# Kernel tuning notes

Hardware: AMD Instinct MI355X
Metric: run time of the kernel (lower is better)

Reference implementation:

```python
import jax, jax.numpy as jnp
import numpy as np

B, W, F_IN = 128, 128, 64   # batch, window_size, num_features
N = 64                      # nodes per graph == num_features == tcn_out_channels
E = 4096                    # edges per graph
ED = 16                     # edge_feature_dim
H, C = 4, 32                # heads, gat_out_dim
FLAT = N * H * C            # 8192
HID = FLAT // 4             # 2048
LRELU_SLOPE = 0.01          # F.leaky_relu default
BN_EPS = 1e-5


def setup_inputs() -> dict:
    key = jax.random.key(0)
    ks = jax.random.split(key, 16)
    x = jax.random.normal(ks[0], (B, W, F_IN), jnp.float32)
    edge_index = jax.random.randint(ks[1], (2, E), 0, N)
    edge_attr = jax.random.normal(ks[2], (B, E, ED), jnp.float32)
    s = lambda k, shape, fan: jax.random.normal(k, shape, jnp.float32) / np.sqrt(fan)
    tcn_w = s(ks[3], (N, F_IN, 3), F_IN * 3)
    tcn_b = jnp.zeros((N,), jnp.float32)
    lin_l_w = s(ks[4], (H * C, W), W)
    lin_l_b = jnp.zeros((H * C,), jnp.float32)
    lin_e_w = s(ks[5], (H * C, ED), ED)
    lin_e_b = jnp.zeros((H * C,), jnp.float32)
    att = s(ks[6], (1, H, C), C)
    fc1_w = s(ks[7], (HID, FLAT), FLAT)
    fc1_b = jnp.zeros((HID,), jnp.float32)
    bn_g = jnp.ones((HID,), jnp.float32)
    bn_b = jnp.zeros((HID,), jnp.float32)
    fc2_w = s(ks[8], (2, HID), HID)
    fc2_b = jnp.zeros((2,), jnp.float32)
    return dict(x=x, edge_index=edge_index, edge_attr=edge_attr,
                tcn_w=tcn_w, tcn_b=tcn_b,
                lin_l_w=lin_l_w, lin_l_b=lin_l_b,
                lin_e_w=lin_e_w, lin_e_b=lin_e_b, att=att,
                fc1_w=fc1_w, fc1_b=fc1_b, bn_g=bn_g, bn_b=bn_b,
                fc2_w=fc2_w, fc2_b=fc2_b)


def reference(x, edge_index, edge_attr, tcn_w, tcn_b,
              lin_l_w, lin_l_b, lin_e_w, lin_e_b, att,
              fc1_w, fc1_b, bn_g, bn_b, fc2_w, fc2_b):
    # TCN: Conv1d(k=3, pad=1) over the window dim
    xt = jnp.transpose(x, (0, 2, 1))  # [B, F_IN, W]
    x_g = jax.lax.conv_general_dilated(
        xt, tcn_w, window_strides=(1,), padding=((1, 1),),
        dimension_numbers=('NCH', 'OIH', 'NCH')) + tcn_b[None, :, None]
    # x_g: [B, N, W] -> per-sample graph with N nodes, W-dim node features

    src, dst = edge_index[0], edge_index[1]

    def gat_one(xn, ea):
        # xn: [N, W], ea: [E, ED]
        h = (xn @ lin_l_w.T + lin_l_b).reshape(N, H, C)
        e = (ea @ lin_e_w.T + lin_e_b).reshape(E, H, C)
        xi = h[dst]               # [E, H, C] target node feats
        xj = h[src]               # [E, H, C] source node feats
        a = jax.nn.leaky_relu(xi + xj + e, LRELU_SLOPE)
        score = jnp.einsum('ehc,ohc->eh', a, att)  # [E, H]
        # segment softmax over edges grouped by destination node
        m = jax.ops.segment_max(score, dst, num_segments=N)
        m = jnp.where(jnp.isfinite(m), m, 0.0)
        ex = jnp.exp(score - m[dst])
        den = jax.ops.segment_sum(ex, dst, num_segments=N)
        alpha = ex / (den[dst] + 1e-16)            # [E, H]
        msg = xj * alpha[:, :, None]               # [E, H, C]
        out = jax.ops.segment_sum(msg, dst, num_segments=N)  # [N, H, C]
        return out.reshape(N, H * C)

    x_gat = jax.vmap(gat_one)(x_g, edge_attr)      # [B, N, H*C]
    x_gat = jax.nn.elu(x_gat)
    x_flat = x_gat.reshape(B, FLAT)

    h1 = x_flat @ fc1_w.T + fc1_b
    # BatchNorm1d in eval mode with fresh running stats (mean=0, var=1)
    h1 = h1 * (bn_g / jnp.sqrt(1.0 + BN_EPS)) + bn_b
    h1 = jax.nn.relu(h1)  # dropout is identity in eval
    logits = h1 @ fc2_w.T + fc2_b
    return logits
```

## Files before the change

### kernel.cpp

```cpp
#include <hip/hip_runtime.h>
#include <math.h>

#define BB   128
#define WW   128
#define FIN  64
#define NNODE 64
#define NE   4096
#define EDIM 16
#define NH   4
#define CDIM 32
#define HC   128
#define FLATD 8192
#define HIDD 2048

#define OFF_H    0u
#define OFF_P    1048576u
#define OFF_XGB  3211264u
#define OFF_BK   4259840u

typedef unsigned short u16;
typedef u16      u16x8 __attribute__((ext_vector_type(8)));
typedef __bf16   bf16x8 __attribute__((ext_vector_type(8)));
typedef float    f32x4  __attribute__((ext_vector_type(4)));
typedef float    f32x16 __attribute__((ext_vector_type(16)));

__device__ __forceinline__ u16 f2bf(float f) {
    unsigned u = __float_as_uint(f);
    u += 0x7fffu + ((u >> 16) & 1u);
    return (u16)(u >> 16);
}
__device__ __forceinline__ void hilo(float v, u16* h, u16* l) {
    u16 hh = f2bf(v);
    float hf = __uint_as_float(((unsigned)hh) << 16);
    *h = hh;
    *l = f2bf(v - hf);
}

__global__ __launch_bounds__(256) void k01(
        const float* __restrict__ x, const float* __restrict__ tcn_w,
        const float* __restrict__ tcn_b, const float* __restrict__ lin_l_w,
        const float* __restrict__ lin_l_b, float* __restrict__ h,
        const int* __restrict__ ei, int* __restrict__ bstart,
        int* __restrict__ blist)
{
    __shared__ float xs[130*65];
    __shared__ float xg[32*132];
    __shared__ float twT[192*32];
    __shared__ int cnt[64];
    __shared__ int cur[65];
    const int bid = blockIdx.x, t = threadIdx.x;

    if (bid == 256) {
        if (t < 64) cnt[t] = 0;
        __syncthreads();
        for (int e = t; e < NE; e += 256) atomicAdd(&cnt[ei[NE + e]], 1);
        __syncthreads();
        if (t == 0) {
            int run = 0;
            for (int n = 0; n < 64; ++n) { cur[n] = run; run += cnt[n]; }
            cur[64] = run;
        }
        __syncthreads();
        if (t < 65) bstart[t] = cur[t];
        __syncthreads();
        for (int e = t; e < NE; e += 256) {
            int d = ei[NE + e], s = ei[e];
            int p = atomicAdd(&cur[d], 1);
            blist[p] = (e << 12) | (d << 6) | s;
        }
        return;
    }

    const int b = bid >> 1, half = bid & 1;
    const int n0 = half * 32;

    for (int idx = t; idx < 8192; idx += 256) {
        int w = idx >> 6, i = idx & 63;
        xs[(w+1)*65 + i] = x[b*8192 + idx];
    }
    for (int idx = t; idx < 6144; idx += 256) {
        const int nl = idx & 31, ik = idx >> 5;
        twT[idx] = tcn_w[(n0 + nl)*192 + ik];
    }
    if (t < 65) { xs[t] = 0.f; xs[129*65 + t] = 0.f; }
    __syncthreads();

    {
        const int nl = t >> 3;
        const int n  = n0 + nl;
        const int w0 = (t & 7) * 16;
        float acc[16];
        const float tb = tcn_b[n];
#pragma unroll
        for (int j = 0; j < 16; ++j) acc[j] = tb;
        for (int i = 0; i < 64; ++i) {
            const float t0 = twT[(3*i + 0)*32 + nl];
            const float t1 = twT[(3*i + 1)*32 + nl];
            const float t2 = twT[(3*i + 2)*32 + nl];
            float a = xs[(w0+0)*65 + i];
            float c0 = xs[(w0+1)*65 + i];
#pragma unroll
            for (int dw = 0; dw < 16; ++dw) {
                float c = xs[(w0+dw+2)*65 + i];
                acc[dw] += a*t0 + c0*t1 + c*t2;
                a = c0; c0 = c;
            }
        }
#pragma unroll
        for (int dw = 0; dw < 16; ++dw) xg[nl*132 + w0 + dw] = acc[dw];
    }
    __syncthreads();

    {
        const int o2 = t & 63, ng = t >> 6;
        const int oA = o2, oB = o2 + 64;
        float accA[8], accB[8];
        const float lbA = lin_l_b[oA], lbB = lin_l_b[oB];
#pragma unroll
        for (int j = 0; j < 8; ++j) { accA[j] = lbA; accB[j] = lbB; }
        for (int c = 0; c < 32; ++c) {
            const float4 lwA = *(const float4*)&lin_l_w[oA*128 + c*4];
            const float4 lwB = *(const float4*)&lin_l_w[oB*128 + c*4];
#pragma unroll
            for (int nn = 0; nn < 8; ++nn) {
                const float4 xv = *(const float4*)&xg[(ng*8+nn)*132 + c*4];
                accA[nn] += xv.x*lwA.x + xv.y*lwA.y + xv.z*lwA.z + xv.w*lwA.w;
                accB[nn] += xv.x*lwB.x + xv.y*lwB.y + xv.z*lwB.z + xv.w*lwB.w;
            }
        }
#pragma unroll
        for (int nn = 0; nn < 8; ++nn) {
            const int n = n0 + ng*8 + nn;
            h[(b*64 + n)*128 + oA] = accA[nn];
            h[(b*64 + n)*128 + oB] = accB[nn];
        }
    }
}

#define CAPF 2560
__global__ __launch_bounds__(512, 1) void k2_fused(
        const float* __restrict__ hbase, const float* __restrict__ ea,
        const float* __restrict__ lin_e_w, const float* __restrict__ lin_e_b,
        const float* __restrict__ att, const int* __restrict__ bstart,
        const int* __restrict__ blist, u16* __restrict__ xgb)
{
    __shared__ float hbuf[64*132];
    __shared__ float scl[CAPF*4];
    __shared__ float Pm[4][32][68];
    __shared__ int   bst[33];
    const int b = blockIdx.x, half = blockIdx.y, t = threadIdx.x;
    const int lane = t & 63, wv = t >> 6, l32 = lane & 31, h5 = lane >> 5;

    const int lo  = bstart[half*32];
    const int cnt = min(bstart[half*32 + 32] - lo, CAPF);
    const int gcnt = (cnt + 31) >> 5;

    int g = wv;
    int pkc = 0; bool validc = false;
    float4 v0c = {0.f,0.f,0.f,0.f}, v1c = {0.f,0.f,0.f,0.f};
    if (g < gcnt) {
        const int idx0 = g*32 + l32;
        validc = idx0 < cnt;
        pkc = validc ? blist[lo + idx0] : 0;
        const float* eap = ea + ((size_t)b*NE + (size_t)(pkc >> 12))*16 + h5*8;
        v0c = *(const float4*)eap;
        v1c = *(const float4*)(eap + 4);
    }

    for (int idx = t; idx < 2048; idx += 512) {
        const int row = idx >> 5, c4 = (idx & 31) * 4;
        float4 hv = *(const float4*)&hbase[(size_t)b*8192 + row*128 + c4];
        const float4 eb = *(const float4*)&lin_e_b[c4];
        hv.x += 0.5f*eb.x; hv.y += 0.5f*eb.y;
        hv.z += 0.5f*eb.z; hv.w += 0.5f*eb.w;
        *(float4*)&hbuf[row*132 + c4] = hv;
    }
    {
        const f32x4 z4 = {0.f, 0.f, 0.f, 0.f};
        for (int idx = t; idx < 4*32*68/4; idx += 512) ((f32x4*)Pm)[idx] = z4;
    }
    if (t < 33) bst[t] = bstart[half*32 + t];
    bf16x8 Ah[4], Al[4];
#pragma unroll
    for (int mt = 0; mt < 4; ++mt) {
        const float* wp = &lin_e_w[(mt*32 + l32)*16 + h5*8];
        const float4 w0 = *(const float4*)wp;
        const float4 w1 = *(const float4*)(wp + 4);
        u16 th[8], tl[8];
        hilo(w0.x,&th[0],&tl[0]); hilo(w0.y,&th[1],&tl[1]);
        hilo(w0.z,&th[2],&tl[2]); hilo(w0.w,&th[3],&tl[3]);
        hilo(w1.x,&th[4],&tl[4]); hilo(w1.y,&th[5],&tl[5]);
        hilo(w1.z,&th[6],&tl[6]); hilo(w1.w,&th[7],&tl[7]);
        u16x8 vh = { th[0],th[1],th[2],th[3],th[4],th[5],th[6],th[7] };
        u16x8 vl = { tl[0],tl[1],tl[2],tl[3],tl[4],tl[5],tl[6],tl[7] };
        Ah[mt] = *(bf16x8*)&vh;
        Al[mt] = *(bf16x8*)&vl;
    }
    float4 attv[4][4];
#pragma unroll
    for (int mt = 0; mt < 4; ++mt)
#pragma unroll
        for (int gq = 0; gq < 4; ++gq)
            attv[mt][gq] = *(const float4*)&att[mt*32 + gq*8 + h5*4];
    __syncthreads();

    while (g < gcnt) {
        const int gn = g + 8;
        const int pk = pkc; const bool valid = validc;
        const float4 v0 = v0c, v1 = v1c;
        const int idx = g*32 + l32;
        if (gn < gcnt) {
            const int idxn = gn*32 + l32;
            validc = idxn < cnt;
            pkc = validc ? blist[lo + idxn] : 0;
            const float* eap = ea + ((size_t)b*NE + (size_t)(pkc >> 12))*16 + h5*8;
            v0c = *(const float4*)eap;
            v1c = *(const float4*)(eap + 4);
        } else {
            validc = false;
        }
        const int sn = pk & 63, dd = (pk >> 6) & 63;
        u16 bh[8], bl[8];
        hilo(v0.x,&bh[0],&bl[0]); hilo(v0.y,&bh[1],&bl[1]);
        hilo(v0.z,&bh[2],&bl[2]); hilo(v0.w,&bh[3],&bl[3]);
        hilo(v1.x,&bh[4],&bl[4]); hilo(v1.y,&bh[5],&bl[5]);
        hilo(v1.z,&bh[6],&bl[6]); hilo(v1.w,&bh[7],&bl[7]);
        u16x8 vbh = { bh[0],bh[1],bh[2],bh[3],bh[4],bh[5],bh[6],bh[7] };
        u16x8 vbl = { bl[0],bl[1],bl[2],bl[3],bl[4],bl[5],bl[6],bl[7] };
        const bf16x8 Bh = *(bf16x8*)&vbh;
        const bf16x8 Bl = *(bf16x8*)&vbl;
        float hacc[4];
#pragma unroll
        for (int mt = 0; mt < 4; ++mt) {
            f32x16 D = {0.f,0.f,0.f,0.f,0.f,0.f,0.f,0.f,
                        0.f,0.f,0.f,0.f,0.f,0.f,0.f,0.f};
            D = __builtin_amdgcn_mfma_f32_32x32x16_bf16(Al[mt], Bh, D, 0, 0, 0);
            D = __builtin_amdgcn_mfma_f32_32x32x16_bf16(Ah[mt], Bl, D, 0, 0, 0);
            D = __builtin_amdgcn_mfma_f32_32x32x16_bf16(Ah[mt], Bh, D, 0, 0, 0);
            float s = 0.f;
#pragma unroll
            for (int g4 = 0; g4 < 4; ++g4) {
                const int ob = mt*32 + g4*8 + h5*4;
                const float4 hd = *(const float4*)&hbuf[dd*132 + ob];
                const float4 hs = *(const float4*)&hbuf[sn*132 + ob];
                float x0 = hd.x + hs.x + D[g4*4+0];
                float x1 = hd.y + hs.y + D[g4*4+1];
                float x2 = hd.z + hs.z + D[g4*4+2];
                float x3 = hd.w + hs.w + D[g4*4+3];
                x0 = fmaxf(x0, 0.01f*x0); x1 = fmaxf(x1, 0.01f*x1);
                x2 = fmaxf(x2, 0.01f*x2); x3 = fmaxf(x3, 0.01f*x3);
                const float4 a4 = attv[mt][g4];
                s += a4.x*x0 + a4.y*x1 + a4.z*x2 + a4.w*x3;
            }
            hacc[mt] = s;
        }
#pragma unroll
        for (int hh = 0; hh < 4; ++hh)
            hacc[hh] += __shfl_xor(hacc[hh], 32);
        if (h5 == 0 && valid)
            *(float4*)&scl[idx*4] = make_float4(hacc[0], hacc[1], hacc[2], hacc[3]);
        g = gn;
    }
    __syncthreads();

    {
        const int pair = t >> 2, sub = t & 3;
        const int nl = pair >> 2, hh = pair & 3;
        const int s0 = bst[nl] - lo, s1 = bst[nl+1] - lo;
        float mx = -3.4e38f;
        for (int i = s0 + sub; i < s1; i += 4) mx = fmaxf(mx, scl[i*4 + hh]);
        mx = fmaxf(mx, __shfl_xor(mx, 1));
        mx = fmaxf(mx, __shfl_xor(mx, 2));
        float den = 0.f;
        for (int i = s0 + sub; i < s1; i += 4) {
            const float ex = __expf(scl[i*4 + hh] - mx);
            scl[i*4 + hh] = ex;
            den += ex;
        }
        den += __shfl_xor(den, 1);
        den += __shfl_xor(den, 2);
        const float rd = 1.0f / (den + 1e-16f);
        for (int i = s0 + sub; i < s1; i += 4) {
            const int src = blist[lo + i] & 63;
            atomicAdd(&Pm[hh][nl][src], scl[i*4 + hh] * rd);
        }
    }
    __syncthreads();

    {
        const int hh = wv >> 1, ct = wv & 1;
        const int l16 = lane & 15, q = lane >> 4;
        const int cb = hh*32 + ct*16 + l16;
        const float lb2 = 0.5f * lin_e_b[cb];
        bf16x8 Hh2[2], Hl2[2];
#pragma unroll
        for (int kk = 0; kk < 2; ++kk) {
            u16 hhv[8], hlv[8];
#pragma unroll
            for (int i = 0; i < 8; ++i) {
                const float v = hbuf[(kk*32 + q*8 + i)*132 + cb];
                hilo(v, &hhv[i], &hlv[i]);
            }
            u16x8 vhh = { hhv[0],hhv[1],hhv[2],hhv[3],hhv[4],hhv[5],hhv[6],hhv[7] };
            u16x8 vhl = { hlv[0],hlv[1],hlv[2],hlv[3],hlv[4],hlv[5],hlv[6],hlv[7] };
            Hh2[kk] = *(bf16x8*)&vhh;
            Hl2[kk] = *(bf16x8*)&vhl;
        }
#pragma unroll
        for (int mrow = 0; mrow < 32; mrow += 16) {
            f32x4 D = {0.f, 0.f, 0.f, 0.f};
#pragma unroll
            for (int kk = 0; kk < 2; ++kk) {
                const float* pp = &Pm[hh][mrow + l16][kk*32 + q*8];
                const float4 a0 = *(const float4*)pp;
                const float4 a1 = *(const float4*)(pp + 4);
                u16 ph[8], pl[8];
                hilo(a0.x,&ph[0],&pl[0]); hilo(a0.y,&ph[1],&pl[1]);
                hilo(a0.z,&ph[2],&pl[2]); hilo(a0.w,&ph[3],&pl[3]);
                hilo(a1.x,&ph[4],&pl[4]); hilo(a1.y,&ph[5],&pl[5]);
                hilo(a1.z,&ph[6],&pl[6]); hilo(a1.w,&ph[7],&pl[7]);
                u16x8 vph = { ph[0],ph[1],ph[2],ph[3],ph[4],ph[5],ph[6],ph[7] };
                u16x8 vpl = { pl[0],pl[1],pl[2],pl[3],pl[4],pl[5],pl[6],pl[7] };
                const bf16x8 Ph = *(bf16x8*)&vph, Pl = *(bf16x8*)&vpl;
                D = __builtin_amdgcn_mfma_f32_16x16x32_bf16(Pl, Hh2[kk], D, 0, 0, 0);
                D = __builtin_amdgcn_mfma_f32_16x16x32_bf16(Ph, Hl2[kk], D, 0, 0, 0);
                D = __builtin_amdgcn_mfma_f32_16x16x32_bf16(Ph, Hh2[kk], D, 0, 0, 0);
            }
#pragma unroll
            for (int r = 0; r < 4; ++r) {
                const int m = mrow + q*4 + r;
                const float corr = (bst[m+1] > bst[m]) ? lb2 : 0.f;
                float v = D[r] - corr;
                v = v > 0.f ? v : expm1f(v);
                xgb[(size_t)b*8192 + (half*32 + m)*128 + cb] = f2bf(v);
            }
        }
    }
}

__global__ __launch_bounds__(256) void k3_fc1(
        const u16* __restrict__ xgb, const float* __restrict__ fc1_w,
        float* __restrict__ part)
{
    __shared__ u16 Ash[2][128*72];
    __shared__ u16 Bsh[2][32*72];
    const int jb = blockIdx.x, ks = blockIdx.y, t = threadIdx.x;
    const int j0 = jb*32, k0 = ks*1024;
    const int wave = t >> 6, lane = t & 63;
    const int quad = lane >> 4, l16 = lane & 15;
    const int wm = (wave & 1) * 64, wn = (wave >> 1) * 16;

    f32x4 acc[4];
#pragma unroll
    for (int i = 0; i < 4; ++i) acc[i] = (f32x4){0.f, 0.f, 0.f, 0.f};

    const int arow = t >> 1, acol = (t & 1) * 32;
    const int brow = t >> 3, bcol = (t & 7) * 8;

#define K3_LOAD(KC, AR, B0, B1)                                              \
    {   const u16* ap = xgb + (size_t)arow*FLATD + k0 + (KC) + acol;         \
        AR[0] = *(const u16x8*)(ap);      AR[1] = *(const u16x8*)(ap + 8);   \
        AR[2] = *(const u16x8*)(ap + 16); AR[3] = *(const u16x8*)(ap + 24);  \
        const float* bp = fc1_w + (size_t)(j0 + brow)*FLATD + k0 + (KC) + bcol; \
        B0 = *(const float4*)bp; B1 = *(const float4*)(bp + 4); }

#define K3_WRITE(BUF, AR, B0, B1)                                            \
    {   *(u16x8*)&Ash[BUF][arow*72 + acol]      = AR[0];                     \
        *(u16x8*)&Ash[BUF][arow*72 + acol + 8]  = AR[1];                     \
        *(u16x8*)&Ash[BUF][arow*72 + acol + 16] = AR[2];                     \
        *(u16x8*)&Ash[BUF][arow*72 + acol + 24] = AR[3];                     \
        u16x8 u = { f2bf(B0.x), f2bf(B0.y), f2bf(B0.z), f2bf(B0.w),          \
                    f2bf(B1.x), f2bf(B1.y), f2bf(B1.z), f2bf(B1.w) };        \
        *(u16x8*)&Bsh[BUF][brow*72 + bcol] = u; }

#define K3_MFMA(BUF)                                                         \
    {   _Pragma("unroll")                                                    \
        for (int kk = 0; kk < 64; kk += 32) {                                \
            bf16x8 af[4], bfr;                                               \
            _Pragma("unroll")                                                \
            for (int i = 0; i < 4; ++i)                                      \
                af[i] = *(const bf16x8*)&Ash[BUF][(wm + i*16 + l16)*72 + kk + quad*8]; \
            bfr = *(const bf16x8*)&Bsh[BUF][(wn + l16)*72 + kk + quad*8];    \
            _Pragma("unroll")                                                \
            for (int i = 0; i < 4; ++i)                                      \
                acc[i] = __builtin_amdgcn_mfma_f32_16x16x32_bf16(af[i], bfr, acc[i], 0, 0, 0); \
        } }

    u16x8 Ar0[4]; float4 B00, B01;
    u16x8 Ar1[4]; float4 B10, B11;

    K3_LOAD(0, Ar0, B00, B01);
    K3_WRITE(0, Ar0, B00, B01);
    K3_LOAD(64, Ar0, B00, B01);
    K3_LOAD(128, Ar1, B10, B11);
    __syncthreads();

    for (int kc = 0; kc < 1024; kc += 128) {
        K3_MFMA(0);
        if (kc + 64 < 1024)  K3_WRITE(1, Ar0, B00, B01);
        if (kc + 192 < 1024) K3_LOAD(kc + 192, Ar0, B00, B01);
        __syncthreads();
        K3_MFMA(1);
        if (kc + 128 < 1024) K3_WRITE(0, Ar1, B10, B11);
        if (kc + 256 < 1024) K3_LOAD(kc + 256, Ar1, B10, B11);
        __syncthreads();
    }
#undef K3_LOAD
#undef K3_WRITE
#undef K3_MFMA

#pragma unroll
    for (int i = 0; i < 4; ++i) {
        const int n = j0 + wn + l16;
#pragma unroll
        for (int r = 0; r < 4; ++r) {
            const int m = wm + i*16 + quad*4 + r;
            part[(size_t)ks*262144 + (size_t)m*HIDD + n] = acc[i][r];
        }
    }
}

__global__ __launch_bounds__(1024) void k4_fc2(
        const float* __restrict__ part, const float* __restrict__ fc1_b,
        const float* __restrict__ bn_g, const float* __restrict__ bn_b,
        const float* __restrict__ fc2_w, const float* __restrict__ fc2_b,
        float* __restrict__ out)
{
    __shared__ float w0s[16], w1s[16];
    const int b = blockIdx.x, t = threadIdx.x;
    const int lane = t & 63, wv = t >> 6;
    const float inv = 1.0f / sqrtf(1.0f + 1e-5f);
    float p0 = 0.f, p1 = 0.f;
#pragma unroll
    for (int jj = 0; jj < 2; ++jj) {
        const int j = t + jj*1024;
        float hv = 0.f;
#pragma unroll
        for (int s = 0; s < 8; ++s) hv += part[(size_t)s*262144 + (size_t)b*2048 + j];
        float v = (hv + fc1_b[j]) * (bn_g[j] * inv) + bn_b[j];
        v = fmaxf(v, 0.f);
        p0 += v * fc2_w[j];
        p1 += v * fc2_w[2048 + j];
    }
#pragma unroll
    for (int d = 1; d < 64; d <<= 1) {
        p0 += __shfl_xor(p0, d);
        p1 += __shfl_xor(p1, d);
    }
    if (lane == 0) { w0s[wv] = p0; w1s[wv] = p1; }
    __syncthreads();
    if (t == 0) {
        float s0 = 0.f, s1 = 0.f;
#pragma unroll
        for (int i = 0; i < 16; ++i) { s0 += w0s[i]; s1 += w1s[i]; }
        out[b*2 + 0] = s0 + fc2_b[0];
        out[b*2 + 1] = s1 + fc2_b[1];
    }
}

extern "C" void kernel_launch(void* const* d_in, const int* in_sizes, int n_in,
                              void* d_out, int out_size, void* d_ws, size_t ws_size,
                              hipStream_t stream)
{
    const float* x       = (const float*)d_in[0];
    const int*   ei      = (const int*)  d_in[1];
    const float* ea      = (const float*)d_in[2];
    const float* tcn_w   = (const float*)d_in[3];
    const float* tcn_b   = (const float*)d_in[4];
    const float* lin_l_w = (const float*)d_in[5];
    const float* lin_l_b = (const float*)d_in[6];
    const float* lin_e_w = (const float*)d_in[7];
    const float* lin_e_b = (const float*)d_in[8];
    const float* att     = (const float*)d_in[9];
    const float* fc1_w   = (const float*)d_in[10];
    const float* fc1_b   = (const float*)d_in[11];
    const float* bn_g    = (const float*)d_in[12];
    const float* bn_b    = (const float*)d_in[13];
    const float* fc2_w   = (const float*)d_in[14];
    const float* fc2_b   = (const float*)d_in[15];

    float* ws     = (float*)d_ws;
    float* hbuf   = ws + OFF_H;
    float* part   = ws + OFF_P;
    u16*   xgb    = (u16*)(ws + OFF_XGB);
    int*   bstart = (int*)(ws + OFF_BK);
    int*   blist  = bstart + 80;
    float* out    = (float*)d_out;

    k01    <<<257, 256, 0, stream>>>(x, tcn_w, tcn_b, lin_l_w, lin_l_b, hbuf,
                                     ei, bstart, blist);
    k2_fused<<<dim3(BB, 2), 512, 0, stream>>>(hbuf, ea, lin_e_w, lin_e_b, att,
                                              bstart, blist, xgb);
    k3_fc1 <<<dim3(64, 8), 256, 0, stream>>>(xgb, fc1_w, part);
    k4_fc2 <<<BB, 1024, 0, stream>>>(part, fc1_b, bn_g, bn_b, fc2_w, fc2_b, out);
}
```

Before: 232.3 us.

## Fuse TCN conv and node projection into GAT kernel, drop global h buffer

The TCN convolution and lin_l projection now run inside the GAT kernel, writing node features straight into shared memory through a union-style shared layout instead of round-tripping through a global buffer. Edge bucketing moves to its own single-block kernel. The aim is to remove the global write and re-read of h and the work split across two launches. The cost is that each of the two blocks per sample (one per half of the destination nodes) now recomputes the full 64-node conv and projection. It also adds 512 threads' worth of extra compute before the edge phase of a kernel that runs at one block per CU.

```diff
diff --git a/kernel.cpp b/kernel.cpp
--- a/kernel.cpp
+++ b/kernel.cpp
@@ -36,118 +36,57 @@
     *l = f2bf(v - hf);
 }
 
-__global__ __launch_bounds__(256) void k01(
+__global__ __launch_bounds__(256) void k0_bucket(
+        const int* __restrict__ ei, int* __restrict__ bstart, int* __restrict__ blist)
+{
+    __shared__ int cnt[64];
+    __shared__ int cur[65];
+    const int t = threadIdx.x;
+    if (t < 64) cnt[t] = 0;
+    __syncthreads();
+    for (int e = t; e < NE; e += 256) atomicAdd(&cnt[ei[NE + e]], 1);
+    __syncthreads();
+    if (t == 0) {
+        int run = 0;
+        for (int n = 0; n < 64; ++n) { cur[n] = run; run += cnt[n]; }
+        cur[64] = run;
+    }
+    __syncthreads();
+    if (t < 65) bstart[t] = cur[t];
+    __syncthreads();
+    for (int e = t; e < NE; e += 256) {
+        int d = ei[NE + e], s = ei[e];
+        int p = atomicAdd(&cur[d], 1);
+        blist[p] = (e << 12) | (d << 6) | s;
+    }
+}
+
+#define CAPF 2560
+#define SM_XG   0u
+#define SM_HB   33792u
+#define SM_XS   33792u
+#define SM_TWT  67600u
+#define SM_SCL  67600u
+#define SM_PM   108560u
+#define SM_BST  143376u
+#define SM_SZ   143512u
+__global__ __launch_bounds__(512, 1) void k2_fused(
         const float* __restrict__ x, const float* __restrict__ tcn_w,
         const float* __restrict__ tcn_b, const float* __restrict__ lin_l_w,
-        const float* __restrict__ lin_l_b, float* __restrict__ h,
-        const int* __restrict__ ei, int* __restrict__ bstart,
-        int* __restrict__ blist)
-{
-    __shared__ float xs[130*65];
-    __shared__ float xg[32*132];
-    __shared__ float twT[192*32];
-    __shared__ int cnt[64];
-    __shared__ int cur[65];
-    const int bid = blockIdx.x, t = threadIdx.x;
-
-    if (bid == 256) {
-        if (t < 64) cnt[t] = 0;
-        __syncthreads();
-        for (int e = t; e < NE; e += 256) atomicAdd(&cnt[ei[NE + e]], 1);
-        __syncthreads();
-        if (t == 0) {
-            int run = 0;
-            for (int n = 0; n < 64; ++n) { cur[n] = run; run += cnt[n]; }
-            cur[64] = run;
-        }
-        __syncthreads();
-        if (t < 65) bstart[t] = cur[t];
-        __syncthreads();
-        for (int e = t; e < NE; e += 256) {
-            int d = ei[NE + e], s = ei[e];
-            int p = atomicAdd(&cur[d], 1);
-            blist[p] = (e << 12) | (d << 6) | s;
-        }
-        return;
-    }
-
-    const int b = bid >> 1, half = bid & 1;
-    const int n0 = half * 32;
-
-    for (int idx = t; idx < 8192; idx += 256) {
-        int w = idx >> 6, i = idx & 63;
-        xs[(w+1)*65 + i] = x[b*8192 + idx];
-    }
-    for (int idx = t; idx < 6144; idx += 256) {
-        const int nl = idx & 31, ik = idx >> 5;
-        twT[idx] = tcn_w[(n0 + nl)*192 + ik];
-    }
-    if (t < 65) { xs[t] = 0.f; xs[129*65 + t] = 0.f; }
-    __syncthreads();
-
-    {
-        const int nl = t >> 3;
-        const int n  = n0 + nl;
-        const int w0 = (t & 7) * 16;
-        float acc[16];
-        const float tb = tcn_b[n];
-#pragma unroll
-        for (int j = 0; j < 16; ++j) acc[j] = tb;
-        for (int i = 0; i < 64; ++i) {
-            const float t0 = twT[(3*i + 0)*32 + nl];
-            const float t1 = twT[(3*i + 1)*32 + nl];
-            const float t2 = twT[(3*i + 2)*32 + nl];
-            float a = xs[(w0+0)*65 + i];
-            float c0 = xs[(w0+1)*65 + i];
-#pragma unroll
-            for (int dw = 0; dw < 16; ++dw) {
-                float c = xs[(w0+dw+2)*65 + i];
-                acc[dw] += a*t0 + c0*t1 + c*t2;
-                a = c0; c0 = c;
-            }
-        }
-#pragma unroll
-        for (int dw = 0; dw < 16; ++dw) xg[nl*132 + w0 + dw] = acc[dw];
-    }
-    __syncthreads();
-
-    {
-        const int o2 = t & 63, ng = t >> 6;
-        const int oA = o2, oB = o2 + 64;
-        float accA[8], accB[8];
-        const float lbA = lin_l_b[oA], lbB = lin_l_b[oB];
-#pragma unroll
-        for (int j = 0; j < 8; ++j) { accA[j] = lbA; accB[j] = lbB; }
-        for (int c = 0; c < 32; ++c) {
-            const float4 lwA = *(const float4*)&lin_l_w[oA*128 + c*4];
-            const float4 lwB = *(const float4*)&lin_l_w[oB*128 + c*4];
-#pragma unroll
-            for (int nn = 0; nn < 8; ++nn) {
-                const float4 xv = *(const float4*)&xg[(ng*8+nn)*132 + c*4];
-                accA[nn] += xv.x*lwA.x + xv.y*lwA.y + xv.z*lwA.z + xv.w*lwA.w;
-                accB[nn] += xv.x*lwB.x + xv.y*lwB.y + xv.z*lwB.z + xv.w*lwB.w;
-            }
-        }
-#pragma unroll
-        for (int nn = 0; nn < 8; ++nn) {
-            const int n = n0 + ng*8 + nn;
-            h[(b*64 + n)*128 + oA] = accA[nn];
-            h[(b*64 + n)*128 + oB] = accB[nn];
-        }
-    }
-}
-
-#define CAPF 2560
-__global__ __launch_bounds__(512, 1) void k2_fused(
-        const float* __restrict__ hbase, const float* __restrict__ ea,
+        const float* __restrict__ lin_l_b, const float* __restrict__ ea,
         const float* __restrict__ lin_e_w, const float* __restrict__ lin_e_b,
         const float* __restrict__ att, const int* __restrict__ bstart,
         const int* __restrict__ blist, u16* __restrict__ xgb)
 {
-    __shared__ float hbuf[64*132];
-    __shared__ float scl[CAPF*4];
-    __shared__ float Pm[4][32][68];
-    __shared__ int   bst[33];
+    __shared__ __align__(16) char smem[SM_SZ];
+    float* xg   = (float*)(smem + SM_XG);
+    float* hbuf = (float*)(smem + SM_HB);
+    float* xs   = (float*)(smem + SM_XS);
+    float* twT  = (float*)(smem + SM_TWT);
+    float* scl  = (float*)(smem + SM_SCL);
+    float* Pm   = (float*)(smem + SM_PM);
+    int*   bst  = (int*)(smem + SM_BST);
+
     const int b = blockIdx.x, half = blockIdx.y, t = threadIdx.x;
     const int lane = t & 63, wv = t >> 6, l32 = lane & 31, h5 = lane >> 5;
 
@@ -167,19 +106,16 @@
         v1c = *(const float4*)(eap + 4);
     }
 
-    for (int idx = t; idx < 2048; idx += 512) {
-        const int row = idx >> 5, c4 = (idx & 31) * 4;
-        float4 hv = *(const float4*)&hbase[(size_t)b*8192 + row*128 + c4];
-        const float4 eb = *(const float4*)&lin_e_b[c4];
-        hv.x += 0.5f*eb.x; hv.y += 0.5f*eb.y;
-        hv.z += 0.5f*eb.z; hv.w += 0.5f*eb.w;
-        *(float4*)&hbuf[row*132 + c4] = hv;
-    }
-    {
-        const f32x4 z4 = {0.f, 0.f, 0.f, 0.f};
-        for (int idx = t; idx < 4*32*68/4; idx += 512) ((f32x4*)Pm)[idx] = z4;
-    }
-    if (t < 33) bst[t] = bstart[half*32 + t];
+    for (int idx = t; idx < 8192; idx += 512) {
+        const int w = idx >> 6, i = idx & 63;
+        xs[(w+1)*65 + i] = x[(size_t)b*8192 + idx];
+    }
+    for (int idx = t; idx < 12288; idx += 512) {
+        const int n = idx & 63, ik = idx >> 6;
+        twT[idx] = tcn_w[n*192 + ik];
+    }
+    if (t < 65) { xs[t] = 0.f; xs[129*65 + t] = 0.f; }
+
     bf16x8 Ah[4], Al[4];
 #pragma unroll
     for (int mt = 0; mt < 4; ++mt) {
@@ -202,6 +138,63 @@
 #pragma unroll
         for (int gq = 0; gq < 4; ++gq)
             attv[mt][gq] = *(const float4*)&att[mt*32 + gq*8 + h5*4];
+    __syncthreads();
+
+    {
+        const int nl = t >> 3;
+        const int w0 = (t & 7) * 16;
+        float acc[16];
+        const float tb = tcn_b[nl];
+#pragma unroll
+        for (int j = 0; j < 16; ++j) acc[j] = tb;
+        for (int i = 0; i < 64; ++i) {
+            const float t0 = twT[(3*i + 0)*64 + nl];
+            const float t1 = twT[(3*i + 1)*64 + nl];
+            const float t2 = twT[(3*i + 2)*64 + nl];
+            float a = xs[(w0+0)*65 + i];
+            float c0 = xs[(w0+1)*65 + i];
+#pragma unroll
+            for (int dw = 0; dw < 16; ++dw) {
+                float c = xs[(w0+dw+2)*65 + i];
+                acc[dw] += a*t0 + c0*t1 + c*t2;
+                a = c0; c0 = c;
+            }
+        }
+#pragma unroll
+        for (int dw = 0; dw < 16; ++dw) xg[nl*132 + w0 + dw] = acc[dw];
+    }
+    __syncthreads();
+
+    {
+        const int o2 = t & 63, ng = t >> 6;
+        const int oA = o2, oB = o2 + 64;
+        float accA[8], accB[8];
+        const float lbA = lin_l_b[oA] + 0.5f*lin_e_b[oA];
+        const float lbB = lin_l_b[oB] + 0.5f*lin_e_b[oB];
+#pragma unroll
+        for (int j = 0; j < 8; ++j) { accA[j] = lbA; accB[j] = lbB; }
+        for (int c = 0; c < 32; ++c) {
+            const float4 lwA = *(const float4*)&lin_l_w[oA*128 + c*4];
+            const float4 lwB = *(const float4*)&lin_l_w[oB*128 + c*4];
+#pragma unroll
+            for (int nn = 0; nn < 8; ++nn) {
+                const float4 xv = *(const float4*)&xg[(ng*8+nn)*132 + c*4];
+                accA[nn] += xv.x*lwA.x + xv.y*lwA.y + xv.z*lwA.z + xv.w*lwA.w;
+                accB[nn] += xv.x*lwB.x + xv.y*lwB.y + xv.z*lwB.z + xv.w*lwB.w;
+            }
+        }
+#pragma unroll
+        for (int nn = 0; nn < 8; ++nn) {
+            const int n = ng*8 + nn;
+            hbuf[n*132 + oA] = accA[nn];
+            hbuf[n*132 + oB] = accB[nn];
+        }
+    }
+    {
+        const f32x4 z4 = {0.f, 0.f, 0.f, 0.f};
+        for (int idx = t; idx < 4*32*68/4; idx += 512) ((f32x4*)Pm)[idx] = z4;
+    }
+    if (t < 33) bst[t] = bstart[half*32 + t];
     __syncthreads();
 
     while (g < gcnt) {
@@ -282,7 +275,7 @@
         const float rd = 1.0f / (den + 1e-16f);
         for (int i = s0 + sub; i < s1; i += 4) {
             const int src = blist[lo + i] & 63;
-            atomicAdd(&Pm[hh][nl][src], scl[i*4 + hh] * rd);
+            atomicAdd(Pm + (hh*32 + nl)*68 + src, scl[i*4 + hh] * rd);
         }
     }
     __syncthreads();
@@ -311,7 +304,7 @@
             f32x4 D = {0.f, 0.f, 0.f, 0.f};
 #pragma unroll
             for (int kk = 0; kk < 2; ++kk) {
-                const float* pp = &Pm[hh][mrow + l16][kk*32 + q*8];
+                const float* pp = Pm + (hh*32 + mrow + l16)*68 + kk*32 + q*8;
                 const float4 a0 = *(const float4*)pp;
                 const float4 a1 = *(const float4*)(pp + 4);
                 u16 ph[8], pl[8];
@@ -480,17 +473,16 @@
     const float* fc2_b   = (const float*)d_in[15];
 
     float* ws     = (float*)d_ws;
-    float* hbuf   = ws + OFF_H;
     float* part   = ws + OFF_P;
     u16*   xgb    = (u16*)(ws + OFF_XGB);
     int*   bstart = (int*)(ws + OFF_BK);
     int*   blist  = bstart + 80;
     float* out    = (float*)d_out;
 
-    k01    <<<257, 256, 0, stream>>>(x, tcn_w, tcn_b, lin_l_w, lin_l_b, hbuf,
-                                     ei, bstart, blist);
-    k2_fused<<<dim3(BB, 2), 512, 0, stream>>>(hbuf, ea, lin_e_w, lin_e_b, att,
-                                              bstart, blist, xgb);
-    k3_fc1 <<<dim3(64, 8), 256, 0, stream>>>(xgb, fc1_w, part);
-    k4_fc2 <<<BB, 1024, 0, stream>>>(part, fc1_b, bn_g, bn_b, fc2_w, fc2_b, out);
-}
+    k0_bucket<<<1, 256, 0, stream>>>(ei, bstart, blist);
+    k2_fused <<<dim3(BB, 2), 512, 0, stream>>>(x, tcn_w, tcn_b, lin_l_w, lin_l_b,
+                                               ea, lin_e_w, lin_e_b, att,
+                                               bstart, blist, xgb);
+    k3_fc1   <<<dim3(64, 8), 256, 0, stream>>>(xgb, fc1_w, part);
+    k4_fc2   <<<BB, 1024, 0, stream>>>(part, fc1_b, bn_g, bn_b, fc2_w, fc2_b, out);
+}
```

Measured after the change: 269.2 us. 1.16x slower.

## Vectorize TCN conv with swizzled LDS and halve fc1 split-K factor

Applied to the files above, without the earlier changes.

The TCN conv in k01 now stores x in a XOR-swizzled padded LDS layout and the weights per node contiguously. This lets each thread read float4 vectors over four input channels and cut LDS instruction count and bank conflicts. Separately, the fc1 split-K goes from 8 to 4 slices of 2048, which halves the partial-sum traffic and the reduction work in fc2 but leaves fewer blocks (256) to fill the GPU. The workspace offsets are compacted to match the smaller partial buffer.

```diff
diff --git a/kernel.cpp b/kernel.cpp
--- a/kernel.cpp
+++ b/kernel.cpp
@@ -15,8 +15,8 @@
 
 #define OFF_H    0u
 #define OFF_P    1048576u
-#define OFF_XGB  3211264u
-#define OFF_BK   4259840u
+#define OFF_XGB  2097152u
+#define OFF_BK   2621440u
 
 typedef unsigned short u16;
 typedef u16      u16x8 __attribute__((ext_vector_type(8)));
@@ -43,9 +43,9 @@
         const int* __restrict__ ei, int* __restrict__ bstart,
         int* __restrict__ blist)
 {
-    __shared__ float xs[130*65];
+    __shared__ float xsw[130*68];
     __shared__ float xg[32*132];
-    __shared__ float twT[192*32];
+    __shared__ float twn[32*3*68];
     __shared__ int cnt[64];
     __shared__ int cur[65];
     const int bid = blockIdx.x, t = threadIdx.x;
@@ -75,35 +75,45 @@
     const int n0 = half * 32;
 
     for (int idx = t; idx < 8192; idx += 256) {
-        int w = idx >> 6, i = idx & 63;
-        xs[(w+1)*65 + i] = x[b*8192 + idx];
+        const int wo = idx >> 6, i = idx & 63;
+        const int row = wo + 1;
+        const int g = (row >> 4) & 7;
+        xsw[row*68 + (((i >> 2) ^ g) << 2) + (i & 3)] = x[b*8192 + idx];
     }
     for (int idx = t; idx < 6144; idx += 256) {
-        const int nl = idx & 31, ik = idx >> 5;
-        twT[idx] = tcn_w[(n0 + nl)*192 + ik];
-    }
-    if (t < 65) { xs[t] = 0.f; xs[129*65 + t] = 0.f; }
+        const int nl = idx / 192, r = idx - nl*192;
+        const int k = r >> 6, i = r & 63;
+        twn[(nl*3 + k)*68 + i] = tcn_w[(n0 + nl)*192 + i*3 + k];
+    }
+    if (t < 68) { xsw[t] = 0.f; xsw[129*68 + t] = 0.f; }
     __syncthreads();
 
     {
         const int nl = t >> 3;
-        const int n  = n0 + nl;
-        const int w0 = (t & 7) * 16;
+        const int G  = t & 7;
+        const int w0 = G * 16;
         float acc[16];
-        const float tb = tcn_b[n];
+        const float tb = tcn_b[n0 + nl];
 #pragma unroll
         for (int j = 0; j < 16; ++j) acc[j] = tb;
-        for (int i = 0; i < 64; ++i) {
-            const float t0 = twT[(3*i + 0)*32 + nl];
-            const float t1 = twT[(3*i + 1)*32 + nl];
-            const float t2 = twT[(3*i + 2)*32 + nl];
-            float a = xs[(w0+0)*65 + i];
-            float c0 = xs[(w0+1)*65 + i];
+        for (int i4 = 0; i4 < 16; ++i4) {
+            const float4 t0v = *(const float4*)&twn[(nl*3 + 0)*68 + i4*4];
+            const float4 t1v = *(const float4*)&twn[(nl*3 + 1)*68 + i4*4];
+            const float4 t2v = *(const float4*)&twn[(nl*3 + 2)*68 + i4*4];
+            float4 r[18];
+#pragma unroll
+            for (int j = 0; j < 18; ++j) {
+                const int gj = (G + (j >= 16 ? 1 : 0)) & 7;
+                r[j] = *(const float4*)&xsw[(w0 + j)*68 + ((i4 ^ gj) << 2)];
+            }
 #pragma unroll
             for (int dw = 0; dw < 16; ++dw) {
-                float c = xs[(w0+dw+2)*65 + i];
-                acc[dw] += a*t0 + c0*t1 + c*t2;
-                a = c0; c0 = c;
+                acc[dw] += r[dw+0].x*t0v.x + r[dw+0].y*t0v.y
+                         + r[dw+0].z*t0v.z + r[dw+0].w*t0v.w
+                         + r[dw+1].x*t1v.x + r[dw+1].y*t1v.y
+                         + r[dw+1].z*t1v.z + r[dw+1].w*t1v.w
+                         + r[dw+2].x*t2v.x + r[dw+2].y*t2v.y
+                         + r[dw+2].z*t2v.z + r[dw+2].w*t2v.w;
             }
         }
 #pragma unroll
@@ -338,6 +348,7 @@
     }
 }
 
+#define KTOT 2048
 __global__ __launch_bounds__(256) void k3_fc1(
         const u16* __restrict__ xgb, const float* __restrict__ fc1_w,
         float* __restrict__ part)
@@ -345,7 +356,7 @@
     __shared__ u16 Ash[2][128*72];
     __shared__ u16 Bsh[2][32*72];
     const int jb = blockIdx.x, ks = blockIdx.y, t = threadIdx.x;
-    const int j0 = jb*32, k0 = ks*1024;
+    const int j0 = jb*32, k0 = ks*KTOT;
     const int wave = t >> 6, lane = t & 63;
     const int quad = lane >> 4, l16 = lane & 15;
     const int wm = (wave & 1) * 64, wn = (wave >> 1) * 16;
@@ -395,14 +406,14 @@
     K3_LOAD(128, Ar1, B10, B11);
     __syncthreads();
 
-    for (int kc = 0; kc < 1024; kc += 128) {
+    for (int kc = 0; kc < KTOT; kc += 128) {
         K3_MFMA(0);
-        if (kc + 64 < 1024)  K3_WRITE(1, Ar0, B00, B01);
-        if (kc + 192 < 1024) K3_LOAD(kc + 192, Ar0, B00, B01);
+        if (kc + 64 < KTOT)  K3_WRITE(1, Ar0, B00, B01);
+        if (kc + 192 < KTOT) K3_LOAD(kc + 192, Ar0, B00, B01);
         __syncthreads();
         K3_MFMA(1);
-        if (kc + 128 < 1024) K3_WRITE(0, Ar1, B10, B11);
-        if (kc + 256 < 1024) K3_LOAD(kc + 256, Ar1, B10, B11);
+        if (kc + 128 < KTOT) K3_WRITE(0, Ar1, B10, B11);
+        if (kc + 256 < KTOT) K3_LOAD(kc + 256, Ar1, B10, B11);
         __syncthreads();
     }
 #undef K3_LOAD
@@ -436,7 +447,7 @@
         const int j = t + jj*1024;
         float hv = 0.f;
 #pragma unroll
-        for (int s = 0; s < 8; ++s) hv += part[(size_t)s*262144 + (size_t)b*2048 + j];
+        for (int s = 0; s < 4; ++s) hv += part[(size_t)s*262144 + (size_t)b*2048 + j];
         float v = (hv + fc1_b[j]) * (bn_g[j] * inv) + bn_b[j];
         v = fmaxf(v, 0.f);
         p0 += v * fc2_w[j];
@@ -487,10 +498,10 @@
     int*   blist  = bstart + 80;
     float* out    = (float*)d_out;
 
-    k01    <<<257, 256, 0, stream>>>(x, tcn_w, tcn_b, lin_l_w, lin_l_b, hbuf,
-                                     ei, bstart, blist);
+    k01     <<<257, 256, 0, stream>>>(x, tcn_w, tcn_b, lin_l_w, lin_l_b, hbuf,
+                                      ei, bstart, blist);
     k2_fused<<<dim3(BB, 2), 512, 0, stream>>>(hbuf, ea, lin_e_w, lin_e_b, att,
                                               bstart, blist, xgb);
-    k3_fc1 <<<dim3(64, 8), 256, 0, stream>>>(xgb, fc1_w, part);
-    k4_fc2 <<<BB, 1024, 0, stream>>>(part, fc1_b, bn_g, bn_b, fc2_w, fc2_b, out);
-}
+    k3_fc1  <<<dim3(64, 4), 256, 0, stream>>>(xgb, fc1_w, part);
+    k4_fc2  <<<BB, 1024, 0, stream>>>(part, fc1_b, bn_g, bn_b, fc2_w, fc2_b, out);
+}
```

Result: faster. 223.7 us, median of 2 (-3.7%).
